# Performance work log

Hardware: AMD Instinct MI355X
Metric: run time of the kernel (lower is better)

Reference implementation:

```python
import jax, jax.numpy as jnp
import numpy as np

N_NODES, N_EDGES, P, C, H = 10000, 80000, 4, 128, 8
D = C // H


def setup_inputs() -> dict:
    key = jax.random.key(0)
    ks = jax.random.split(key, 24)

    def lin(k, i, o):
        return (jax.random.normal(k, (i, o), jnp.float32) / np.sqrt(i)).astype(jnp.float32)

    return {
        'h': jax.random.normal(ks[0], (N_NODES, P, C), jnp.float32),
        'e': jax.random.normal(ks[1], (N_EDGES, P, C), jnp.float32),
        'src': jax.random.randint(ks[2], (N_EDGES,), 0, N_NODES),
        'dst': jax.random.randint(ks[3], (N_EDGES,), 0, N_NODES),
        # MultiHeadAttentionLayer (use_bias=False)
        'Wq': lin(ks[4], C, C), 'Wk': lin(ks[5], C, C), 'Wv': lin(ks[6], C, C), 'We': lin(ks[7], C, C),
        # EnhanceLayer (bias=False)
        'eWq': lin(ks[8], C, C), 'eWk': lin(ks[9], C, C), 'eWv': lin(ks[10], C, C), 'eWre': lin(ks[11], C, C),
        # output projections
        'Oh_w': lin(ks[12], C, C), 'Oh_b': jnp.zeros((C,), jnp.float32),
        'Oe_w': lin(ks[13], C, C), 'Oe_b': jnp.zeros((C,), jnp.float32),
        # batch-norm affine params (training-mode stats)
        'bn_h_g': jnp.ones((C,), jnp.float32), 'bn_h_b': jnp.zeros((C,), jnp.float32),
        'bn_e_g': jnp.ones((C,), jnp.float32), 'bn_e_b': jnp.zeros((C,), jnp.float32),
        # FFN for h
        'W1': lin(ks[14], C, 2 * C), 'b1': jnp.zeros((2 * C,), jnp.float32),
        'W2': lin(ks[15], 2 * C, C), 'b2': jnp.zeros((C,), jnp.float32),
    }


def _forward(h, e, src, dst, Wq, Wk, Wv, We, eWq, eWk, eWv, eWre,
             Oh_w, Oh_b, Oe_w, Oe_b, bn_h_g, bn_h_b, bn_e_g, bn_e_b,
             W1, b1, W2, b2):
    n_nodes, p, c = h.shape
    n_edges = src.shape[0]
    d = c // H

    def heads(x):
        return x.reshape(x.shape[0], p, H, d)

    # ---- MultiHeadAttentionLayer.propagate_attention ----
    Q = heads(h @ Wq)          # (n, P, H, D)
    K = heads(h @ Wk)
    V = heads(h @ Wv)
    proj_e = heads(e @ We)     # (E, P, H, D)

    # src_dot_dst -> scaling -> relative_pe_attn
    score = (K[src] * Q[dst]) / jnp.sqrt(jnp.float32(d)) + proj_e  # (E, P, H, D)
    e_out = score                                                  # out_edge_features('score')
    s = jnp.exp(jnp.clip(score.sum(-1, keepdims=True), -5.0, 5.0))  # (E, P, H, 1)

    wV = jax.ops.segment_sum(V[src] * s, dst, num_segments=n_nodes)  # (n, P, H, D)
    z = jax.ops.segment_sum(s, dst, num_segments=n_nodes)            # (n, P, H, 1)
    h_attn = wV / (z + 1e-6)

    # ---- EnhanceLayer.propagate_attention ----
    Qe = heads(h @ eWq)
    diff = jax.nn.relu(h[src] - h[dst])             # (E, P, C)
    k_diff = heads(diff @ eWk)                      # (E, P, H, D)
    v_diff = heads(diff @ eWv)
    repe = heads(e @ eWre)
    qd = Qe[dst]
    # dst_cosim_diff: (q*k) * (||k||*||q|| + 1e-6) + repe   (eps in sqrt for grad safety)
    nk = jnp.sqrt(jnp.sum(k_diff * k_diff, -1, keepdims=True) + 1e-12)
    nq = jnp.sqrt(jnp.sum(qd * qd, -1, keepdims=True) + 1e-12)
    sc = qd * k_diff * (nk * nq + 1e-6) + repe
    msg = sc * v_diff
    h_enh = jax.ops.segment_max(msg, dst, num_segments=n_nodes)
    h_enh = jnp.where(jnp.isfinite(h_enh), h_enh, 0.0)  # DGL zero-fills nodes with no in-edges

    # ---- combine, project, residual, BN, FFN (dropout=0) ----
    hf = (h_attn + h_enh).reshape(n_nodes * p, c)
    ef = e_out.reshape(n_edges * p, c)
    hf = hf @ Oh_w + Oh_b
    ef = ef @ Oe_w + Oe_b
    hf = h.reshape(-1, c) + hf   # residual
    ef = e.reshape(-1, c) + ef

    def bn(x, g, b):
        m = x.mean(0)
        v = x.var(0)
        return (x - m) * jax.lax.rsqrt(v + 1e-5) * g + b

    hf = bn(hf, bn_h_g, bn_h_b)
    ef = bn(ef, bn_e_g, bn_e_b)

    h2 = hf
    hf = jax.nn.relu(hf @ W1 + b1) @ W2 + b2
    hf = h2 + hf
    return hf.reshape(n_nodes, p, c), ef.reshape(n_edges, p, c)


def reference(h, e, src, dst, Wq, Wk, Wv, We, eWq, eWk, eWv, eWre,
              Oh_w, Oh_b, Oe_w, Oe_b, bn_h_g, bn_h_b, bn_e_g, bn_e_b,
              W1, b1, W2, b2):
    return _forward(h, e, src, dst, Wq, Wk, Wv, We, eWq, eWk, eWv, eWre,
                    Oh_w, Oh_b, Oe_w, Oe_b, bn_h_g, bn_h_b, bn_e_g, bn_e_b,
                    W1, b1, W2, b2)
```

## Files before the change

kernel.cpp:

```cpp
#include <hip/hip_runtime.h>
#include <hip/hip_bf16.h>

#define NN 10000
#define NE 80000
#define PP 4
#define CC 128
#define NR (NN*PP)
#define ER (NE*PP)
#define S1 136
#define S2 264

typedef unsigned short u16;
typedef unsigned int   u32;
typedef __attribute__((ext_vector_type(8))) short short8;
typedef __attribute__((ext_vector_type(4))) float f32x4;

__device__ inline float b2f(u16 v) { return __uint_as_float(((u32)v) << 16); }
__device__ inline u16 f2b(float f) {
    u32 x = __float_as_uint(f);
    return (u16)((x + 0x7fffu + ((x >> 16) & 1u)) >> 16);
}
__device__ inline void atomicMaxF(float* addr, float val) {
    if (val >= 0.f) atomicMax((int*)addr, __float_as_int(val));
    else            atomicMin((u32*)addr, __float_as_uint(val));
}
__device__ inline f32x4 mfma16(short8 a, short8 b, f32x4 c) {
    return __builtin_amdgcn_mfma_f32_16x16x32_bf16(a, b, c, 0, 0, 0);
}

__global__ __launch_bounds__(512) void k_qkvqe(const float* __restrict__ h,
    const float* __restrict__ Wq, const float* __restrict__ Wk,
    const float* __restrict__ Wv, const float* __restrict__ eWq,
    float* __restrict__ out)
{
    __shared__ __align__(16) u16 hH[64 * S1];
    __shared__ __align__(16) u16 hL[64 * S1];
    const int t = threadIdx.x;
    const int lane = t & 63;
    const int wid = t >> 6;
    const int lrow = lane & 15;
    const int lgrp = lane >> 4;

    short8 wf[4][4];
#pragma unroll
    for (int nt = 0; nt < 4; ++nt) {
        int col = wid * 64 + nt * 16 + lrow;
        int sel = col >> 7, wc = col & 127;
        const float* W = (sel == 0) ? Wq : (sel == 1) ? Wk : (sel == 2) ? Wv : eWq;
#pragma unroll
        for (int ks = 0; ks < 4; ++ks) {
            short8 a;
#pragma unroll
            for (int j = 0; j < 8; ++j) {
                int k = ks * 32 + lgrp * 8 + j;
                a[j] = (short)f2b(W[k * 128 + wc]);
            }
            wf[nt][ks] = a;
        }
    }

    const int nTiles = NR / 64;
    for (int tl = blockIdx.x; tl < nTiles; tl += gridDim.x) {
        const int rbase = tl * 64;
        {
            int r = t >> 3, c0 = (t & 7) * 16;
            const float4* h4 = (const float4*)(h + (size_t)(rbase + r) * 128 + c0);
            u32* HH = (u32*)(hH + r * S1 + c0);
            u32* HL = (u32*)(hL + r * S1 + c0);
#pragma unroll
            for (int q2 = 0; q2 < 4; ++q2) {
                float4 v = h4[q2];
                u16 h0 = f2b(v.x), h1 = f2b(v.y), h2 = f2b(v.z), h3 = f2b(v.w);
                HH[q2 * 2]     = (u32)h0 | ((u32)h1 << 16);
                HH[q2 * 2 + 1] = (u32)h2 | ((u32)h3 << 16);
                u16 l0 = f2b(v.x - b2f(h0)), l1 = f2b(v.y - b2f(h1));
                u16 l2 = f2b(v.z - b2f(h2)), l3 = f2b(v.w - b2f(h3));
                HL[q2 * 2]     = (u32)l0 | ((u32)l1 << 16);
                HL[q2 * 2 + 1] = (u32)l2 | ((u32)l3 << 16);
            }
        }
        __syncthreads();
#pragma unroll
        for (int mt = 0; mt < 4; ++mt) {
            short8 Hh[4], Hl[4];
#pragma unroll
            for (int ks = 0; ks < 4; ++ks) {
                const int off = (mt * 16 + lrow) * S1 + ks * 32 + lgrp * 8;
                Hh[ks] = *(const short8*)(hH + off);
                Hl[ks] = *(const short8*)(hL + off);
            }
#pragma unroll
            for (int nt = 0; nt < 4; ++nt) {
                f32x4 acc = {0.f, 0.f, 0.f, 0.f};
#pragma unroll
                for (int ks = 0; ks < 4; ++ks) {
                    acc = mfma16(Hh[ks], wf[nt][ks], acc);
                    acc = mfma16(Hl[ks], wf[nt][ks], acc);
                }
#pragma unroll
                for (int q = 0; q < 4; ++q) {
                    int r = rbase + mt * 16 + lgrp * 4 + q;
                    out[(size_t)r * 512 + wid * 64 + nt * 16 + lrow] = acc[q];
                }
            }
        }
        __syncthreads();
    }
}

__global__ __launch_bounds__(512, 4) void k_attn(const float* __restrict__ e,
    const int* __restrict__ src, const int* __restrict__ dst,
    const float* __restrict__ We, const float* __restrict__ Oe_w, const float* __restrict__ Oe_b,
    const float* __restrict__ qkvqe, float* __restrict__ wV, float* __restrict__ z,
    float* __restrict__ stats, float* __restrict__ out_e)
{
    __shared__ __align__(16) u16 eH[64 * S1];
    __shared__ __align__(16) u16 eL[64 * S1];
    __shared__ int drowS[64], srowS[64];

    const int t = threadIdx.x;
    const int lane = t & 63;
    const int wid = t >> 6;
    const int lrow = lane & 15;
    const int lgrp = lane >> 4;
    const int c = wid * 16 + lrow;

    short8 we8[4], oe8[4];
#pragma unroll
    for (int ks = 0; ks < 4; ++ks) {
        short8 a, b;
#pragma unroll
        for (int j = 0; j < 8; ++j) {
            int k = ks * 32 + lgrp * 8 + j;
            int idx = k * 128 + c;
            a[j] = (short)f2b(We[idx]);
            b[j] = (short)f2b(Oe_w[idx]);
        }
        we8[ks] = a; oe8[ks] = b;
    }
    const float oeb = Oe_b[c];
    float s1 = 0.f, s2 = 0.f;

    const int nTiles = ER / 64;
    for (int tl = blockIdx.x; tl < nTiles; tl += gridDim.x) {
        const int rbase = tl * 64;
        {
            int r = t >> 3, c0 = (t & 7) * 16;
            int re = rbase + r, ei = re >> 2, p = re & 3;
            if ((t & 7) == 0) { drowS[r] = dst[ei] * 4 + p; srowS[r] = src[ei] * 4 + p; }
            const float4* ee4 = (const float4*)(e + (size_t)re * 128 + c0);
            u32* EH = (u32*)(eH + r * S1 + c0);
            u32* EL = (u32*)(eL + r * S1 + c0);
#pragma unroll
            for (int q2 = 0; q2 < 4; ++q2) {
                float4 ev = ee4[q2];
                u16 e0 = f2b(ev.x), e1 = f2b(ev.y), e2 = f2b(ev.z), e3 = f2b(ev.w);
                EH[q2 * 2]     = (u32)e0 | ((u32)e1 << 16);
                EH[q2 * 2 + 1] = (u32)e2 | ((u32)e3 << 16);
                u16 g0 = f2b(ev.x - b2f(e0)), g1 = f2b(ev.y - b2f(e1));
                u16 g2 = f2b(ev.z - b2f(e2)), g3 = f2b(ev.w - b2f(e3));
                EL[q2 * 2]     = (u32)g0 | ((u32)g1 << 16);
                EL[q2 * 2 + 1] = (u32)g2 | ((u32)g3 << 16);
            }
        }
        __syncthreads();

        f32x4 ap0 = {0.f,0.f,0.f,0.f}, ap1 = {0.f,0.f,0.f,0.f};
        f32x4 ap2 = {0.f,0.f,0.f,0.f}, ap3 = {0.f,0.f,0.f,0.f};
#pragma unroll
        for (int ks = 0; ks < 4; ++ks) {
            const int boff = ks * 32 + lgrp * 8;
            ap0 = mfma16(*(const short8*)(eH + (0 * 16 + lrow) * S1 + boff), we8[ks], ap0);
            ap0 = mfma16(*(const short8*)(eL + (0 * 16 + lrow) * S1 + boff), we8[ks], ap0);
            ap1 = mfma16(*(const short8*)(eH + (1 * 16 + lrow) * S1 + boff), we8[ks], ap1);
            ap1 = mfma16(*(const short8*)(eL + (1 * 16 + lrow) * S1 + boff), we8[ks], ap1);
            ap2 = mfma16(*(const short8*)(eH + (2 * 16 + lrow) * S1 + boff), we8[ks], ap2);
            ap2 = mfma16(*(const short8*)(eL + (2 * 16 + lrow) * S1 + boff), we8[ks], ap2);
            ap3 = mfma16(*(const short8*)(eH + (3 * 16 + lrow) * S1 + boff), we8[ks], ap3);
            ap3 = mfma16(*(const short8*)(eL + (3 * 16 + lrow) * S1 + boff), we8[ks], ap3);
        }
        __syncthreads();

        float evr[16];
#pragma unroll
        for (int mt = 0; mt < 4; ++mt) {
            int dr4[4], sr4[4];
#pragma unroll
            for (int q = 0; q < 4; ++q) {
                int rr = mt * 16 + lgrp * 4 + q;
                dr4[q] = drowS[rr]; sr4[q] = srowS[rr];
            }
            float kg[4], qg[4], vg[4];
#pragma unroll
            for (int q = 0; q < 4; ++q) {
                kg[q] = qkvqe[(size_t)sr4[q] * 512 + 128 + c];
                qg[q] = qkvqe[(size_t)dr4[q] * 512 + c];
                vg[q] = qkvqe[(size_t)sr4[q] * 512 + 256 + c];
            }
            f32x4 ap = (mt == 0) ? ap0 : (mt == 1) ? ap1 : (mt == 2) ? ap2 : ap3;
#pragma unroll
            for (int q = 0; q < 4; ++q) {
                int rr = mt * 16 + lgrp * 4 + q;
                float scv = kg[q] * qg[q] * 0.25f + ap[q];
                float hs = scv;
                hs += __shfl_xor(hs, 1); hs += __shfl_xor(hs, 2);
                hs += __shfl_xor(hs, 4); hs += __shfl_xor(hs, 8);
                hs = fminf(fmaxf(hs, -5.f), 5.f);
                float sv = expf(hs);
                if (lrow == 0) atomicAdd(&z[dr4[q] * 8 + wid], sv);
                atomicAdd(&wV[(size_t)dr4[q] * 128 + c], vg[q] * sv);
                int off2 = rr * S1 + c;
                evr[mt * 4 + q] = b2f(eH[off2]) + b2f(eL[off2]);
                u16 shh = f2b(scv);
                eH[off2] = shh;
                eL[off2] = f2b(scv - b2f(shh));
            }
        }
        __syncthreads();

#pragma unroll
        for (int mt = 0; mt < 4; ++mt) {
            f32x4 ao = {0.f, 0.f, 0.f, 0.f};
#pragma unroll
            for (int ks = 0; ks < 4; ++ks) {
                const int off = (mt * 16 + lrow) * S1 + ks * 32 + lgrp * 8;
                ao = mfma16(*(const short8*)(eH + off), oe8[ks], ao);
                ao = mfma16(*(const short8*)(eL + off), oe8[ks], ao);
            }
#pragma unroll
            for (int q = 0; q < 4; ++q) {
                int rr = mt * 16 + lgrp * 4 + q;
                int re = rbase + rr;
                float ef = evr[mt * 4 + q] + oeb + ao[q];
                out_e[(size_t)re * 128 + c] = ef;
                s1 += ef; s2 += ef * ef;
            }
        }
        __syncthreads();
    }
    atomicAdd(&stats[256 + c], s1);
    atomicAdd(&stats[384 + c], s2);
}

__global__ __launch_bounds__(512) void k_enh(const float* __restrict__ h, const float* __restrict__ e,
    const int* __restrict__ src, const int* __restrict__ dst,
    const float* __restrict__ eWk, const float* __restrict__ eWv, const float* __restrict__ eWre,
    const float* __restrict__ qkvqe, float* __restrict__ henh)
{
    __shared__ __align__(16) u16 diffH[64 * S1];
    __shared__ __align__(16) u16 diffL[64 * S1];
    __shared__ __align__(16) u16 erH[64 * S1];
    __shared__ __align__(16) u16 erL[64 * S1];
    __shared__ int drowS[64];

    const int t = threadIdx.x;
    const int lane = t & 63;
    const int wid = t >> 6;
    const int lrow = lane & 15;
    const int lgrp = lane >> 4;

    short8 wkh[4], wkl[4], wv8[4], wre8[4];
#pragma unroll
    for (int ks = 0; ks < 4; ++ks) {
        short8 a, b, c2, d2;
#pragma unroll
        for (int j = 0; j < 8; ++j) {
            int k = ks * 32 + lgrp * 8 + j;
            int idx = k * 128 + wid * 16 + lrow;
            float wk = eWk[idx];
            u16 hh = f2b(wk);
            a[j]  = (short)hh;
            b[j]  = (short)f2b(wk - b2f(hh));
            c2[j] = (short)f2b(eWv[idx]);
            d2[j] = (short)f2b(eWre[idx]);
        }
        wkh[ks] = a; wkl[ks] = b; wv8[ks] = c2; wre8[ks] = d2;
    }

    const int nTiles = ER / 64;
    for (int tl = blockIdx.x; tl < nTiles; tl += gridDim.x) {
        const int rbase = tl * 64;
        {
            int r = t >> 3, c0 = (t & 7) * 16;
            int re = rbase + r, ei = re >> 2, p = re & 3;
            int sr = src[ei] * 4 + p, dr = dst[ei] * 4 + p;
            if ((t & 7) == 0) drowS[r] = dr;
            const float4* hs4 = (const float4*)(h + (size_t)sr * 128 + c0);
            const float4* hd4 = (const float4*)(h + (size_t)dr * 128 + c0);
            const float4* ee4 = (const float4*)(e + (size_t)re * 128 + c0);
            u32* dH = (u32*)(diffH + r * S1 + c0);
            u32* dL = (u32*)(diffL + r * S1 + c0);
            u32* eH = (u32*)(erH + r * S1 + c0);
            u32* eL = (u32*)(erL + r * S1 + c0);
#pragma unroll
            for (int q2 = 0; q2 < 4; ++q2) {
                float4 a = hs4[q2], b = hd4[q2], ev = ee4[q2];
                float d0 = fmaxf(a.x - b.x, 0.f), d1 = fmaxf(a.y - b.y, 0.f);
                float d2 = fmaxf(a.z - b.z, 0.f), d3 = fmaxf(a.w - b.w, 0.f);
                u16 h0 = f2b(d0), h1 = f2b(d1), h2 = f2b(d2), h3 = f2b(d3);
                dH[q2 * 2]     = (u32)h0 | ((u32)h1 << 16);
                dH[q2 * 2 + 1] = (u32)h2 | ((u32)h3 << 16);
                u16 l0 = f2b(d0 - b2f(h0)), l1 = f2b(d1 - b2f(h1));
                u16 l2 = f2b(d2 - b2f(h2)), l3 = f2b(d3 - b2f(h3));
                dL[q2 * 2]     = (u32)l0 | ((u32)l1 << 16);
                dL[q2 * 2 + 1] = (u32)l2 | ((u32)l3 << 16);
                u16 e0 = f2b(ev.x), e1 = f2b(ev.y), e2 = f2b(ev.z), e3 = f2b(ev.w);
                eH[q2 * 2]     = (u32)e0 | ((u32)e1 << 16);
                eH[q2 * 2 + 1] = (u32)e2 | ((u32)e3 << 16);
                u16 g0 = f2b(ev.x - b2f(e0)), g1 = f2b(ev.y - b2f(e1));
                u16 g2 = f2b(ev.z - b2f(e2)), g3 = f2b(ev.w - b2f(e3));
                eL[q2 * 2]     = (u32)g0 | ((u32)g1 << 16);
                eL[q2 * 2 + 1] = (u32)g2 | ((u32)g3 << 16);
            }
        }
        __syncthreads();

#pragma unroll
        for (int mt = 0; mt < 4; ++mt) {
            f32x4 ak = {0.f, 0.f, 0.f, 0.f};
            f32x4 av = {0.f, 0.f, 0.f, 0.f};
            f32x4 ar = {0.f, 0.f, 0.f, 0.f};
#pragma unroll
            for (int ks = 0; ks < 4; ++ks) {
                const int off = (mt * 16 + lrow) * S1 + ks * 32 + lgrp * 8;
                short8 Ah = *(const short8*)(diffH + off);
                short8 Al = *(const short8*)(diffL + off);
                short8 Eh = *(const short8*)(erH + off);
                short8 El = *(const short8*)(erL + off);
                ak = mfma16(Ah, wkh[ks], ak);
                ak = mfma16(Al, wkh[ks], ak);
                ak = mfma16(Ah, wkl[ks], ak);
                av = mfma16(Ah, wv8[ks], av);
                av = mfma16(Al, wv8[ks], av);
                ar = mfma16(Eh, wre8[ks], ar);
                ar = mfma16(El, wre8[ks], ar);
            }
#pragma unroll
            for (int q = 0; q < 4; ++q) {
                int rr = mt * 16 + lgrp * 4 + q;
                int dr = drowS[rr];
                float qd = qkvqe[(size_t)dr * 512 + 384 + wid * 16 + lrow];
                float kd = ak[q];
                float sk = kd * kd;
                sk += __shfl_xor(sk, 1); sk += __shfl_xor(sk, 2);
                sk += __shfl_xor(sk, 4); sk += __shfl_xor(sk, 8);
                float sq = qd * qd;
                sq += __shfl_xor(sq, 1); sq += __shfl_xor(sq, 2);
                sq += __shfl_xor(sq, 4); sq += __shfl_xor(sq, 8);
                float nk = sqrtf(sk + 1e-12f);
                float nq = sqrtf(sq + 1e-12f);
                float sc = qd * kd * (nk * nq + 1e-6f) + ar[q];
                float msg = sc * av[q];
                atomicMaxF(&henh[(size_t)dr * 128 + wid * 16 + lrow], msg);
            }
        }
        __syncthreads();
    }
}

__global__ __launch_bounds__(512, 8) void k_comb(const float* __restrict__ h,
    const float* __restrict__ Oh_w, const float* __restrict__ Oh_b,
    const float* __restrict__ wV, const float* __restrict__ z, const float* __restrict__ henh,
    float* __restrict__ hf, float* __restrict__ stats)
{
    __shared__ __align__(16) u16 xH[64 * S1];
    __shared__ __align__(16) u16 xL[64 * S1];
    const int t = threadIdx.x;
    const int lane = t & 63;
    const int wid = t >> 6;
    const int lrow = lane & 15;
    const int lgrp = lane >> 4;
    const int c = wid * 16 + lrow;

    short8 oh8[4];
#pragma unroll
    for (int ks = 0; ks < 4; ++ks) {
        short8 a;
#pragma unroll
        for (int j = 0; j < 8; ++j) {
            int k = ks * 32 + lgrp * 8 + j;
            a[j] = (short)f2b(Oh_w[k * 128 + c]);
        }
        oh8[ks] = a;
    }
    const float ohb = Oh_b[c];
    float s1 = 0.f, s2 = 0.f;

    const int nTiles = NR / 64;
    for (int tl = blockIdx.x; tl < nTiles; tl += gridDim.x) {
        const int rbase = tl * 64;
        {
            int r = t >> 3, c0 = (t & 7) * 16;
            int gr = rbase + r;
            float zv = z[gr * 8 + (t & 7)] + 1e-6f;
            const float4* wv4 = (const float4*)(wV + (size_t)gr * 128 + c0);
            const float4* he4 = (const float4*)(henh + (size_t)gr * 128 + c0);
            u32* XH = (u32*)(xH + r * S1 + c0);
            u32* XL = (u32*)(xL + r * S1 + c0);
#pragma unroll
            for (int q2 = 0; q2 < 4; ++q2) {
                float4 a = wv4[q2], b = he4[q2];
                float x0, x1, x2, x3;
                {
                    u32 hb = __float_as_uint(b.x); float hv = (((hb >> 23) & 0xffu) == 0xffu) ? 0.f : b.x;
                    x0 = a.x / zv + hv;
                }
                {
                    u32 hb = __float_as_uint(b.y); float hv = (((hb >> 23) & 0xffu) == 0xffu) ? 0.f : b.y;
                    x1 = a.y / zv + hv;
                }
                {
                    u32 hb = __float_as_uint(b.z); float hv = (((hb >> 23) & 0xffu) == 0xffu) ? 0.f : b.z;
                    x2 = a.z / zv + hv;
                }
                {
                    u32 hb = __float_as_uint(b.w); float hv = (((hb >> 23) & 0xffu) == 0xffu) ? 0.f : b.w;
                    x3 = a.w / zv + hv;
                }
                u16 h0 = f2b(x0), h1 = f2b(x1), h2 = f2b(x2), h3 = f2b(x3);
                XH[q2 * 2]     = (u32)h0 | ((u32)h1 << 16);
                XH[q2 * 2 + 1] = (u32)h2 | ((u32)h3 << 16);
                u16 l0 = f2b(x0 - b2f(h0)), l1 = f2b(x1 - b2f(h1));
                u16 l2 = f2b(x2 - b2f(h2)), l3 = f2b(x3 - b2f(h3));
                XL[q2 * 2]     = (u32)l0 | ((u32)l1 << 16);
                XL[q2 * 2 + 1] = (u32)l2 | ((u32)l3 << 16);
            }
        }
        __syncthreads();
#pragma unroll
        for (int mt = 0; mt < 4; ++mt) {
            f32x4 acc = {0.f, 0.f, 0.f, 0.f};
#pragma unroll
            for (int ks = 0; ks < 4; ++ks) {
                const int off = (mt * 16 + lrow) * S1 + ks * 32 + lgrp * 8;
                acc = mfma16(*(const short8*)(xH + off), oh8[ks], acc);
                acc = mfma16(*(const short8*)(xL + off), oh8[ks], acc);
            }
#pragma unroll
            for (int q = 0; q < 4; ++q) {
                int r = rbase + mt * 16 + lgrp * 4 + q;
                float val = h[(size_t)r * 128 + c] + ohb + acc[q];
                hf[(size_t)r * 128 + c] = val;
                s1 += val; s2 += val * val;
            }
        }
        __syncthreads();
    }
    atomicAdd(&stats[c], s1);
    atomicAdd(&stats[128 + c], s2);
}

__global__ void k_bnprep(const float* __restrict__ stats,
    const float* __restrict__ gh, const float* __restrict__ bh,
    const float* __restrict__ ge, const float* __restrict__ be, float* __restrict__ bnsc)
{
    int c = threadIdx.x;
    if (c < 128) {
        float m = stats[c] / (float)NR;
        float v = stats[128 + c] / (float)NR - m * m;
        float sc = gh[c] * rsqrtf(v + 1e-5f);
        bnsc[c] = sc; bnsc[128 + c] = bh[c] - m * sc;
        m = stats[256 + c] / (float)ER;
        v = stats[384 + c] / (float)ER - m * m;
        sc = ge[c] * rsqrtf(v + 1e-5f);
        bnsc[256 + c] = sc; bnsc[384 + c] = be[c] - m * sc;
    }
}

__global__ __launch_bounds__(512, 4) void k_ffn(const float* __restrict__ hf,
    const float* __restrict__ W1, const float* __restrict__ b1,
    const float* __restrict__ W2, const float* __restrict__ b2,
    const float* __restrict__ bnsc, float* __restrict__ out_h)
{
    __shared__ __align__(16) u16 xH[32 * S1];
    __shared__ __align__(16) u16 xL[32 * S1];
    __shared__ __align__(16) u16 tH[32 * S2];
    __shared__ __align__(16) u16 tL[32 * S2];
    __shared__ float scs[128], shs[128];
    const int t = threadIdx.x;
    const int lane = t & 63;
    const int wid = t >> 6;
    const int lrow = lane & 15;
    const int lgrp = lane >> 4;

    short8 w1f[2][4];
#pragma unroll
    for (int nt = 0; nt < 2; ++nt) {
        int col = wid * 32 + nt * 16 + lrow;
#pragma unroll
        for (int ks = 0; ks < 4; ++ks) {
            short8 a;
#pragma unroll
            for (int j = 0; j < 8; ++j) {
                int k = ks * 32 + lgrp * 8 + j;
                a[j] = (short)f2b(W1[k * 256 + col]);
            }
            w1f[nt][ks] = a;
        }
    }
    short8 w2f[8];
#pragma unroll
    for (int ks = 0; ks < 8; ++ks) {
        short8 a;
#pragma unroll
        for (int j = 0; j < 8; ++j) {
            int k = ks * 32 + lgrp * 8 + j;
            a[j] = (short)f2b(W2[k * 128 + wid * 16 + lrow]);
        }
        w2f[ks] = a;
    }
    const float bb1a = b1[wid * 32 + lrow];
    const float bb1b = b1[wid * 32 + 16 + lrow];
    const float bb2 = b2[wid * 16 + lrow];
    if (t < 128) { scs[t] = bnsc[t]; shs[t] = bnsc[128 + t]; }
    __syncthreads();

    const int nTiles = NR / 32;
    for (int tl = blockIdx.x; tl < nTiles; tl += gridDim.x) {
        const int rbase = tl * 32;
        {
            int r = t >> 4, c0 = (t & 15) * 8;
            const float4* s4 = (const float4*)(hf + (size_t)(rbase + r) * 128 + c0);
            u32* XH = (u32*)(xH + r * S1 + c0);
            u32* XL = (u32*)(xL + r * S1 + c0);
#pragma unroll
            for (int q2 = 0; q2 < 2; ++q2) {
                float4 v = s4[q2];
                float x0 = v.x * scs[c0 + q2 * 4 + 0] + shs[c0 + q2 * 4 + 0];
                float x1 = v.y * scs[c0 + q2 * 4 + 1] + shs[c0 + q2 * 4 + 1];
                float x2 = v.z * scs[c0 + q2 * 4 + 2] + shs[c0 + q2 * 4 + 2];
                float x3 = v.w * scs[c0 + q2 * 4 + 3] + shs[c0 + q2 * 4 + 3];
                u16 h0 = f2b(x0), h1 = f2b(x1), h2 = f2b(x2), h3 = f2b(x3);
                XH[q2 * 2]     = (u32)h0 | ((u32)h1 << 16);
                XH[q2 * 2 + 1] = (u32)h2 | ((u32)h3 << 16);
                u16 l0 = f2b(x0 - b2f(h0)), l1 = f2b(x1 - b2f(h1));
                u16 l2 = f2b(x2 - b2f(h2)), l3 = f2b(x3 - b2f(h3));
                XL[q2 * 2]     = (u32)l0 | ((u32)l1 << 16);
                XL[q2 * 2 + 1] = (u32)l2 | ((u32)l3 << 16);
            }
        }
        __syncthreads();
#pragma unroll
        for (int mt = 0; mt < 2; ++mt) {
#pragma unroll
            for (int nt = 0; nt < 2; ++nt) {
                f32x4 acc = {0.f, 0.f, 0.f, 0.f};
#pragma unroll
                for (int ks = 0; ks < 4; ++ks) {
                    const int off = (mt * 16 + lrow) * S1 + ks * 32 + lgrp * 8;
                    acc = mfma16(*(const short8*)(xH + off), w1f[nt][ks], acc);
                    acc = mfma16(*(const short8*)(xL + off), w1f[nt][ks], acc);
                }
                float bb = nt ? bb1b : bb1a;
                int col = wid * 32 + nt * 16 + lrow;
#pragma unroll
                for (int q = 0; q < 4; ++q) {
                    int rr = mt * 16 + lgrp * 4 + q;
                    float tv = fmaxf(acc[q] + bb, 0.f);
                    u16 hh = f2b(tv);
                    tH[rr * S2 + col] = hh;
                    tL[rr * S2 + col] = f2b(tv - b2f(hh));
                }
            }
        }
        __syncthreads();
#pragma unroll
        for (int mt = 0; mt < 2; ++mt) {
            f32x4 acc = {0.f, 0.f, 0.f, 0.f};
#pragma unroll
            for (int ks = 0; ks < 8; ++ks) {
                const int off = (mt * 16 + lrow) * S2 + ks * 32 + lgrp * 8;
                acc = mfma16(*(const short8*)(tH + off), w2f[ks], acc);
                acc = mfma16(*(const short8*)(tL + off), w2f[ks], acc);
            }
            int c2 = wid * 16 + lrow;
#pragma unroll
            for (int q = 0; q < 4; ++q) {
                int rr = mt * 16 + lgrp * 4 + q;
                int offx = rr * S1 + c2;
                float xn = b2f(xH[offx]) + b2f(xL[offx]);
                float o = xn + bb2 + acc[q];
                out_h[(size_t)(rbase + rr) * 128 + c2] = o;
            }
        }
        __syncthreads();
    }
}

__global__ __launch_bounds__(256) void k_bne(float* __restrict__ out_e, const float* __restrict__ bnsc)
{
    __shared__ float scs[128], shs[128];
    const int t = threadIdx.x;
    if (t < 128) { scs[t] = bnsc[256 + t]; shs[t] = bnsc[384 + t]; }
    __syncthreads();
    int idx = blockIdx.x * 256 + t;
    const int total = ER * 128 / 4;
    for (; idx < total; idx += gridDim.x * 256) {
        float4 v = ((const float4*)out_e)[idx];
        int c0 = (idx * 4) & 127;
        v.x = v.x * scs[c0 + 0] + shs[c0 + 0];
        v.y = v.y * scs[c0 + 1] + shs[c0 + 1];
        v.z = v.z * scs[c0 + 2] + shs[c0 + 2];
        v.w = v.w * scs[c0 + 3] + shs[c0 + 3];
        ((float4*)out_e)[idx] = v;
    }
}

extern "C" void kernel_launch(void* const* d_in, const int* in_sizes, int n_in,
                              void* d_out, int out_size, void* d_ws, size_t ws_size,
                              hipStream_t stream)
{
    const float* h    = (const float*)d_in[0];
    const float* e    = (const float*)d_in[1];
    const int* src    = (const int*)d_in[2];
    const int* dst    = (const int*)d_in[3];
    const float* Wq   = (const float*)d_in[4];
    const float* Wk   = (const float*)d_in[5];
    const float* Wv   = (const float*)d_in[6];
    const float* We   = (const float*)d_in[7];
    const float* eWq  = (const float*)d_in[8];
    const float* eWk  = (const float*)d_in[9];
    const float* eWv  = (const float*)d_in[10];
    const float* eWre = (const float*)d_in[11];
    const float* Oh_w = (const float*)d_in[12];
    const float* Oh_b = (const float*)d_in[13];
    const float* Oe_w = (const float*)d_in[14];
    const float* Oe_b = (const float*)d_in[15];
    const float* bnhg = (const float*)d_in[16];
    const float* bnhb = (const float*)d_in[17];
    const float* bneg = (const float*)d_in[18];
    const float* bneb = (const float*)d_in[19];
    const float* W1   = (const float*)d_in[20];
    const float* b1   = (const float*)d_in[21];
    const float* W2   = (const float*)d_in[22];
    const float* b2   = (const float*)d_in[23];

    float* out_h = (float*)d_out;
    float* out_e = out_h + (size_t)NR * 128;

    char* w = (char*)d_ws;
    float* qkvqe = (float*)(w);
    float* wV    = (float*)(w + 81920000);
    float* z     = (float*)(w + 102400000);
    float* henh  = (float*)(w + 103680000);
    float* hf    = (float*)(w + 124160000);
    float* stats = (float*)(w + 144640000);
    float* bnsc  = (float*)(w + 144642048);

    hipMemsetAsync(wV,    0,    20480000, stream);
    hipMemsetAsync(z,     0,    1280000,  stream);
    hipMemsetAsync(stats, 0,    2048,     stream);
    hipMemsetAsync(henh,  0xFF, 20480000, stream);

    k_qkvqe<<<625, 512, 0, stream>>>(h, Wq, Wk, Wv, eWq, qkvqe);
    k_attn <<<1024, 512, 0, stream>>>(e, src, dst, We, Oe_w, Oe_b, qkvqe, wV, z, stats, out_e);
    k_enh  <<<1024, 512, 0, stream>>>(h, e, src, dst, eWk, eWv, eWre, qkvqe, henh);
    k_comb <<<625, 512, 0, stream>>>(h, Oh_w, Oh_b, wV, z, henh, hf, stats);
    k_bnprep<<<1, 128, 0, stream>>>(stats, bnhg, bnhb, bneg, bneb, bnsc);
    k_ffn  <<<1250, 512, 0, stream>>>(hf, W1, b1, W2, b2, bnsc, out_h);
    k_bne  <<<2048, 256, 0, stream>>>(out_e, bnsc);
}
```

Before: 1.582 ms.

## Merge attention and enhance edge kernels into one launch with block-parity split

The two edge-pass kernels are combined into one kernel. Even blocks run the attention/score path and odd blocks run the enhance/segment-max path, so both independent workloads run at the same time on the GPU and fill idle tail slots. Grid size changes to 2000 (1000 blocks per path). The cost is higher shared-memory use (four buffers in every block, which the attention blocks do not need), and this may lower occupancy for the attention half.

```diff
diff --git a/kernel.cpp b/kernel.cpp
--- a/kernel.cpp
+++ b/kernel.cpp
@@ -108,14 +108,18 @@
     }
 }
 
-__global__ __launch_bounds__(512, 4) void k_attn(const float* __restrict__ e,
+__global__ __launch_bounds__(512, 4) void k_edge(
+    const float* __restrict__ h, const float* __restrict__ e,
     const int* __restrict__ src, const int* __restrict__ dst,
     const float* __restrict__ We, const float* __restrict__ Oe_w, const float* __restrict__ Oe_b,
+    const float* __restrict__ eWk, const float* __restrict__ eWv, const float* __restrict__ eWre,
     const float* __restrict__ qkvqe, float* __restrict__ wV, float* __restrict__ z,
-    float* __restrict__ stats, float* __restrict__ out_e)
+    float* __restrict__ stats, float* __restrict__ out_e, float* __restrict__ henh)
 {
-    __shared__ __align__(16) u16 eH[64 * S1];
-    __shared__ __align__(16) u16 eL[64 * S1];
+    __shared__ __align__(16) u16 bAH[64 * S1];
+    __shared__ __align__(16) u16 bAL[64 * S1];
+    __shared__ __align__(16) u16 bBH[64 * S1];
+    __shared__ __align__(16) u16 bBL[64 * S1];
     __shared__ int drowS[64], srowS[64];
 
     const int t = threadIdx.x;
@@ -124,237 +128,222 @@
     const int lrow = lane & 15;
     const int lgrp = lane >> 4;
     const int c = wid * 16 + lrow;
-
-    short8 we8[4], oe8[4];
-#pragma unroll
-    for (int ks = 0; ks < 4; ++ks) {
-        short8 a, b;
-#pragma unroll
-        for (int j = 0; j < 8; ++j) {
-            int k = ks * 32 + lgrp * 8 + j;
-            int idx = k * 128 + c;
-            a[j] = (short)f2b(We[idx]);
-            b[j] = (short)f2b(Oe_w[idx]);
-        }
-        we8[ks] = a; oe8[ks] = b;
-    }
-    const float oeb = Oe_b[c];
-    float s1 = 0.f, s2 = 0.f;
-
+    const int bstream = blockIdx.x >> 1;
     const int nTiles = ER / 64;
-    for (int tl = blockIdx.x; tl < nTiles; tl += gridDim.x) {
-        const int rbase = tl * 64;
-        {
-            int r = t >> 3, c0 = (t & 7) * 16;
-            int re = rbase + r, ei = re >> 2, p = re & 3;
-            if ((t & 7) == 0) { drowS[r] = dst[ei] * 4 + p; srowS[r] = src[ei] * 4 + p; }
-            const float4* ee4 = (const float4*)(e + (size_t)re * 128 + c0);
-            u32* EH = (u32*)(eH + r * S1 + c0);
-            u32* EL = (u32*)(eL + r * S1 + c0);
-#pragma unroll
-            for (int q2 = 0; q2 < 4; ++q2) {
-                float4 ev = ee4[q2];
-                u16 e0 = f2b(ev.x), e1 = f2b(ev.y), e2 = f2b(ev.z), e3 = f2b(ev.w);
-                EH[q2 * 2]     = (u32)e0 | ((u32)e1 << 16);
-                EH[q2 * 2 + 1] = (u32)e2 | ((u32)e3 << 16);
-                u16 g0 = f2b(ev.x - b2f(e0)), g1 = f2b(ev.y - b2f(e1));
-                u16 g2 = f2b(ev.z - b2f(e2)), g3 = f2b(ev.w - b2f(e3));
-                EL[q2 * 2]     = (u32)g0 | ((u32)g1 << 16);
-                EL[q2 * 2 + 1] = (u32)g2 | ((u32)g3 << 16);
-            }
-        }
-        __syncthreads();
-
-        f32x4 ap0 = {0.f,0.f,0.f,0.f}, ap1 = {0.f,0.f,0.f,0.f};
-        f32x4 ap2 = {0.f,0.f,0.f,0.f}, ap3 = {0.f,0.f,0.f,0.f};
+    const int bstride = gridDim.x >> 1;
+
+    if ((blockIdx.x & 1) == 0) {
+        short8 we8[4], oe8[4];
 #pragma unroll
         for (int ks = 0; ks < 4; ++ks) {
-            const int boff = ks * 32 + lgrp * 8;
-            ap0 = mfma16(*(const short8*)(eH + (0 * 16 + lrow) * S1 + boff), we8[ks], ap0);
-            ap0 = mfma16(*(const short8*)(eL + (0 * 16 + lrow) * S1 + boff), we8[ks], ap0);
-            ap1 = mfma16(*(const short8*)(eH + (1 * 16 + lrow) * S1 + boff), we8[ks], ap1);
-            ap1 = mfma16(*(const short8*)(eL + (1 * 16 + lrow) * S1 + boff), we8[ks], ap1);
-            ap2 = mfma16(*(const short8*)(eH + (2 * 16 + lrow) * S1 + boff), we8[ks], ap2);
-            ap2 = mfma16(*(const short8*)(eL + (2 * 16 + lrow) * S1 + boff), we8[ks], ap2);
-            ap3 = mfma16(*(const short8*)(eH + (3 * 16 + lrow) * S1 + boff), we8[ks], ap3);
-            ap3 = mfma16(*(const short8*)(eL + (3 * 16 + lrow) * S1 + boff), we8[ks], ap3);
-        }
-        __syncthreads();
-
-        float evr[16];
-#pragma unroll
-        for (int mt = 0; mt < 4; ++mt) {
-            int dr4[4], sr4[4];
-#pragma unroll
-            for (int q = 0; q < 4; ++q) {
-                int rr = mt * 16 + lgrp * 4 + q;
-                dr4[q] = drowS[rr]; sr4[q] = srowS[rr];
-            }
-            float kg[4], qg[4], vg[4];
-#pragma unroll
-            for (int q = 0; q < 4; ++q) {
-                kg[q] = qkvqe[(size_t)sr4[q] * 512 + 128 + c];
-                qg[q] = qkvqe[(size_t)dr4[q] * 512 + c];
-                vg[q] = qkvqe[(size_t)sr4[q] * 512 + 256 + c];
-            }
-            f32x4 ap = (mt == 0) ? ap0 : (mt == 1) ? ap1 : (mt == 2) ? ap2 : ap3;
-#pragma unroll
-            for (int q = 0; q < 4; ++q) {
-                int rr = mt * 16 + lgrp * 4 + q;
-                float scv = kg[q] * qg[q] * 0.25f + ap[q];
-                float hs = scv;
-                hs += __shfl_xor(hs, 1); hs += __shfl_xor(hs, 2);
-                hs += __shfl_xor(hs, 4); hs += __shfl_xor(hs, 8);
-                hs = fminf(fmaxf(hs, -5.f), 5.f);
-                float sv = expf(hs);
-                if (lrow == 0) atomicAdd(&z[dr4[q] * 8 + wid], sv);
-                atomicAdd(&wV[(size_t)dr4[q] * 128 + c], vg[q] * sv);
-                int off2 = rr * S1 + c;
-                evr[mt * 4 + q] = b2f(eH[off2]) + b2f(eL[off2]);
-                u16 shh = f2b(scv);
-                eH[off2] = shh;
-                eL[off2] = f2b(scv - b2f(shh));
-            }
-        }
-        __syncthreads();
-
-#pragma unroll
-        for (int mt = 0; mt < 4; ++mt) {
-            f32x4 ao = {0.f, 0.f, 0.f, 0.f};
+            short8 a, b;
+#pragma unroll
+            for (int j = 0; j < 8; ++j) {
+                int k = ks * 32 + lgrp * 8 + j;
+                int idx = k * 128 + c;
+                a[j] = (short)f2b(We[idx]);
+                b[j] = (short)f2b(Oe_w[idx]);
+            }
+            we8[ks] = a; oe8[ks] = b;
+        }
+        const float oeb = Oe_b[c];
+        float s1 = 0.f, s2 = 0.f;
+
+        for (int tl = bstream; tl < nTiles; tl += bstride) {
+            const int rbase = tl * 64;
+            {
+                int r = t >> 3, c0 = (t & 7) * 16;
+                int re = rbase + r, ei = re >> 2, p = re & 3;
+                if ((t & 7) == 0) { drowS[r] = dst[ei] * 4 + p; srowS[r] = src[ei] * 4 + p; }
+                const float4* ee4 = (const float4*)(e + (size_t)re * 128 + c0);
+                u32* EH = (u32*)(bAH + r * S1 + c0);
+                u32* EL = (u32*)(bAL + r * S1 + c0);
+#pragma unroll
+                for (int q2 = 0; q2 < 4; ++q2) {
+                    float4 ev = ee4[q2];
+                    u16 e0 = f2b(ev.x), e1 = f2b(ev.y), e2 = f2b(ev.z), e3 = f2b(ev.w);
+                    EH[q2 * 2]     = (u32)e0 | ((u32)e1 << 16);
+                    EH[q2 * 2 + 1] = (u32)e2 | ((u32)e3 << 16);
+                    u16 g0 = f2b(ev.x - b2f(e0)), g1 = f2b(ev.y - b2f(e1));
+                    u16 g2 = f2b(ev.z - b2f(e2)), g3 = f2b(ev.w - b2f(e3));
+                    EL[q2 * 2]     = (u32)g0 | ((u32)g1 << 16);
+                    EL[q2 * 2 + 1] = (u32)g2 | ((u32)g3 << 16);
+                }
+            }
+            __syncthreads();
+
+            f32x4 ap0 = {0.f,0.f,0.f,0.f}, ap1 = {0.f,0.f,0.f,0.f};
+            f32x4 ap2 = {0.f,0.f,0.f,0.f}, ap3 = {0.f,0.f,0.f,0.f};
 #pragma unroll
             for (int ks = 0; ks < 4; ++ks) {
-                const int off = (mt * 16 + lrow) * S1 + ks * 32 + lgrp * 8;
-                ao = mfma16(*(const short8*)(eH + off), oe8[ks], ao);
-                ao = mfma16(*(const short8*)(eL + off), oe8[ks], ao);
-            }
-#pragma unroll
-            for (int q = 0; q < 4; ++q) {
-                int rr = mt * 16 + lgrp * 4 + q;
-                int re = rbase + rr;
-                float ef = evr[mt * 4 + q] + oeb + ao[q];
-                out_e[(size_t)re * 128 + c] = ef;
-                s1 += ef; s2 += ef * ef;
-            }
-        }
-        __syncthreads();
-    }
-    atomicAdd(&stats[256 + c], s1);
-    atomicAdd(&stats[384 + c], s2);
-}
-
-__global__ __launch_bounds__(512) void k_enh(const float* __restrict__ h, const float* __restrict__ e,
-    const int* __restrict__ src, const int* __restrict__ dst,
-    const float* __restrict__ eWk, const float* __restrict__ eWv, const float* __restrict__ eWre,
-    const float* __restrict__ qkvqe, float* __restrict__ henh)
-{
-    __shared__ __align__(16) u16 diffH[64 * S1];
-    __shared__ __align__(16) u16 diffL[64 * S1];
-    __shared__ __align__(16) u16 erH[64 * S1];
-    __shared__ __align__(16) u16 erL[64 * S1];
-    __shared__ int drowS[64];
-
-    const int t = threadIdx.x;
-    const int lane = t & 63;
-    const int wid = t >> 6;
-    const int lrow = lane & 15;
-    const int lgrp = lane >> 4;
-
-    short8 wkh[4], wkl[4], wv8[4], wre8[4];
-#pragma unroll
-    for (int ks = 0; ks < 4; ++ks) {
-        short8 a, b, c2, d2;
-#pragma unroll
-        for (int j = 0; j < 8; ++j) {
-            int k = ks * 32 + lgrp * 8 + j;
-            int idx = k * 128 + wid * 16 + lrow;
-            float wk = eWk[idx];
-            u16 hh = f2b(wk);
-            a[j]  = (short)hh;
-            b[j]  = (short)f2b(wk - b2f(hh));
-            c2[j] = (short)f2b(eWv[idx]);
-            d2[j] = (short)f2b(eWre[idx]);
-        }
-        wkh[ks] = a; wkl[ks] = b; wv8[ks] = c2; wre8[ks] = d2;
-    }
-
-    const int nTiles = ER / 64;
-    for (int tl = blockIdx.x; tl < nTiles; tl += gridDim.x) {
-        const int rbase = tl * 64;
-        {
-            int r = t >> 3, c0 = (t & 7) * 16;
-            int re = rbase + r, ei = re >> 2, p = re & 3;
-            int sr = src[ei] * 4 + p, dr = dst[ei] * 4 + p;
-            if ((t & 7) == 0) drowS[r] = dr;
-            const float4* hs4 = (const float4*)(h + (size_t)sr * 128 + c0);
-            const float4* hd4 = (const float4*)(h + (size_t)dr * 128 + c0);
-            const float4* ee4 = (const float4*)(e + (size_t)re * 128 + c0);
-            u32* dH = (u32*)(diffH + r * S1 + c0);
-            u32* dL = (u32*)(diffL + r * S1 + c0);
-            u32* eH = (u32*)(erH + r * S1 + c0);
-            u32* eL = (u32*)(erL + r * S1 + c0);
-#pragma unroll
-            for (int q2 = 0; q2 < 4; ++q2) {
-                float4 a = hs4[q2], b = hd4[q2], ev = ee4[q2];
-                float d0 = fmaxf(a.x - b.x, 0.f), d1 = fmaxf(a.y - b.y, 0.f);
-                float d2 = fmaxf(a.z - b.z, 0.f), d3 = fmaxf(a.w - b.w, 0.f);
-                u16 h0 = f2b(d0), h1 = f2b(d1), h2 = f2b(d2), h3 = f2b(d3);
-                dH[q2 * 2]     = (u32)h0 | ((u32)h1 << 16);
-                dH[q2 * 2 + 1] = (u32)h2 | ((u32)h3 << 16);
-                u16 l0 = f2b(d0 - b2f(h0)), l1 = f2b(d1 - b2f(h1));
-                u16 l2 = f2b(d2 - b2f(h2)), l3 = f2b(d3 - b2f(h3));
-                dL[q2 * 2]     = (u32)l0 | ((u32)l1 << 16);
-                dL[q2 * 2 + 1] = (u32)l2 | ((u32)l3 << 16);
-                u16 e0 = f2b(ev.x), e1 = f2b(ev.y), e2 = f2b(ev.z), e3 = f2b(ev.w);
-                eH[q2 * 2]     = (u32)e0 | ((u32)e1 << 16);
-                eH[q2 * 2 + 1] = (u32)e2 | ((u32)e3 << 16);
-                u16 g0 = f2b(ev.x - b2f(e0)), g1 = f2b(ev.y - b2f(e1));
-                u16 g2 = f2b(ev.z - b2f(e2)), g3 = f2b(ev.w - b2f(e3));
-                eL[q2 * 2]     = (u32)g0 | ((u32)g1 << 16);
-                eL[q2 * 2 + 1] = (u32)g2 | ((u32)g3 << 16);
-            }
-        }
-        __syncthreads();
-
-#pragma unroll
-        for (int mt = 0; mt < 4; ++mt) {
-            f32x4 ak = {0.f, 0.f, 0.f, 0.f};
-            f32x4 av = {0.f, 0.f, 0.f, 0.f};
-            f32x4 ar = {0.f, 0.f, 0.f, 0.f};
-#pragma unroll
-            for (int ks = 0; ks < 4; ++ks) {
-                const int off = (mt * 16 + lrow) * S1 + ks * 32 + lgrp * 8;
-                short8 Ah = *(const short8*)(diffH + off);
-                short8 Al = *(const short8*)(diffL + off);
-                short8 Eh = *(const short8*)(erH + off);
-                short8 El = *(const short8*)(erL + off);
-                ak = mfma16(Ah, wkh[ks], ak);
-                ak = mfma16(Al, wkh[ks], ak);
-                ak = mfma16(Ah, wkl[ks], ak);
-                av = mfma16(Ah, wv8[ks], av);
-                av = mfma16(Al, wv8[ks], av);
-                ar = mfma16(Eh, wre8[ks], ar);
-                ar = mfma16(El, wre8[ks], ar);
-            }
-#pragma unroll
-            for (int q = 0; q < 4; ++q) {
-                int rr = mt * 16 + lgrp * 4 + q;
-                int dr = drowS[rr];
-                float qd = qkvqe[(size_t)dr * 512 + 384 + wid * 16 + lrow];
-                float kd = ak[q];
-                float sk = kd * kd;
-                sk += __shfl_xor(sk, 1); sk += __shfl_xor(sk, 2);
-                sk += __shfl_xor(sk, 4); sk += __shfl_xor(sk, 8);
-                float sq = qd * qd;
-                sq += __shfl_xor(sq, 1); sq += __shfl_xor(sq, 2);
-                sq += __shfl_xor(sq, 4); sq += __shfl_xor(sq, 8);
-                float nk = sqrtf(sk + 1e-12f);
-                float nq = sqrtf(sq + 1e-12f);
-                float sc = qd * kd * (nk * nq + 1e-6f) + ar[q];
-                float msg = sc * av[q];
-                atomicMaxF(&henh[(size_t)dr * 128 + wid * 16 + lrow], msg);
-            }
-        }
-        __syncthreads();
+                const int boff = ks * 32 + lgrp * 8;
+                ap0 = mfma16(*(const short8*)(bAH + (0 * 16 + lrow) * S1 + boff), we8[ks], ap0);
+                ap0 = mfma16(*(const short8*)(bAL + (0 * 16 + lrow) * S1 + boff), we8[ks], ap0);
+                ap1 = mfma16(*(const short8*)(bAH + (1 * 16 + lrow) * S1 + boff), we8[ks], ap1);
+                ap1 = mfma16(*(const short8*)(bAL + (1 * 16 + lrow) * S1 + boff), we8[ks], ap1);
+                ap2 = mfma16(*(const short8*)(bAH + (2 * 16 + lrow) * S1 + boff), we8[ks], ap2);
+                ap2 = mfma16(*(const short8*)(bAL + (2 * 16 + lrow) * S1 + boff), we8[ks], ap2);
+                ap3 = mfma16(*(const short8*)(bAH + (3 * 16 + lrow) * S1 + boff), we8[ks], ap3);
+                ap3 = mfma16(*(const short8*)(bAL + (3 * 16 + lrow) * S1 + boff), we8[ks], ap3);
+            }
+            __syncthreads();
+
+            float evr[16];
+#pragma unroll
+            for (int mt = 0; mt < 4; ++mt) {
+                int dr4[4], sr4[4];
+#pragma unroll
+                for (int q = 0; q < 4; ++q) {
+                    int rr = mt * 16 + lgrp * 4 + q;
+                    dr4[q] = drowS[rr]; sr4[q] = srowS[rr];
+                }
+                float kg[4], qg[4], vg[4];
+#pragma unroll
+                for (int q = 0; q < 4; ++q) {
+                    kg[q] = qkvqe[(size_t)sr4[q] * 512 + 128 + c];
+                    qg[q] = qkvqe[(size_t)dr4[q] * 512 + c];
+                    vg[q] = qkvqe[(size_t)sr4[q] * 512 + 256 + c];
+                }
+                f32x4 ap = (mt == 0) ? ap0 : (mt == 1) ? ap1 : (mt == 2) ? ap2 : ap3;
+#pragma unroll
+                for (int q = 0; q < 4; ++q) {
+                    int rr = mt * 16 + lgrp * 4 + q;
+                    float scv = kg[q] * qg[q] * 0.25f + ap[q];
+                    float hs = scv;
+                    hs += __shfl_xor(hs, 1); hs += __shfl_xor(hs, 2);
+                    hs += __shfl_xor(hs, 4); hs += __shfl_xor(hs, 8);
+                    hs = fminf(fmaxf(hs, -5.f), 5.f);
+                    float sv = expf(hs);
+                    if (lrow == 0) atomicAdd(&z[dr4[q] * 8 + wid], sv);
+                    atomicAdd(&wV[(size_t)dr4[q] * 128 + c], vg[q] * sv);
+                    int off2 = rr * S1 + c;
+                    evr[mt * 4 + q] = b2f(bAH[off2]) + b2f(bAL[off2]);
+                    u16 shh = f2b(scv);
+                    bAH[off2] = shh;
+                    bAL[off2] = f2b(scv - b2f(shh));
+                }
+            }
+            __syncthreads();
+
+#pragma unroll
+            for (int mt = 0; mt < 4; ++mt) {
+                f32x4 ao = {0.f, 0.f, 0.f, 0.f};
+#pragma unroll
+                for (int ks = 0; ks < 4; ++ks) {
+                    const int off = (mt * 16 + lrow) * S1 + ks * 32 + lgrp * 8;
+                    ao = mfma16(*(const short8*)(bAH + off), oe8[ks], ao);
+                    ao = mfma16(*(const short8*)(bAL + off), oe8[ks], ao);
+                }
+#pragma unroll
+                for (int q = 0; q < 4; ++q) {
+                    int rr = mt * 16 + lgrp * 4 + q;
+                    int re = rbase + rr;
+                    float ef = evr[mt * 4 + q] + oeb + ao[q];
+                    out_e[(size_t)re * 128 + c] = ef;
+                    s1 += ef; s2 += ef * ef;
+                }
+            }
+            __syncthreads();
+        }
+        atomicAdd(&stats[256 + c], s1);
+        atomicAdd(&stats[384 + c], s2);
+    } else {
+        short8 wkh[4], wkl[4], wv8[4], wre8[4];
+#pragma unroll
+        for (int ks = 0; ks < 4; ++ks) {
+            short8 a, b, c2, d2;
+#pragma unroll
+            for (int j = 0; j < 8; ++j) {
+                int k = ks * 32 + lgrp * 8 + j;
+                int idx = k * 128 + c;
+                float wk = eWk[idx];
+                u16 hh = f2b(wk);
+                a[j]  = (short)hh;
+                b[j]  = (short)f2b(wk - b2f(hh));
+                c2[j] = (short)f2b(eWv[idx]);
+                d2[j] = (short)f2b(eWre[idx]);
+            }
+            wkh[ks] = a; wkl[ks] = b; wv8[ks] = c2; wre8[ks] = d2;
+        }
+
+        for (int tl = bstream; tl < nTiles; tl += bstride) {
+            const int rbase = tl * 64;
+            {
+                int r = t >> 3, c0 = (t & 7) * 16;
+                int re = rbase + r, ei = re >> 2, p = re & 3;
+                int sr = src[ei] * 4 + p, dr = dst[ei] * 4 + p;
+                if ((t & 7) == 0) drowS[r] = dr;
+                const float4* hs4 = (const float4*)(h + (size_t)sr * 128 + c0);
+                const float4* hd4 = (const float4*)(h + (size_t)dr * 128 + c0);
+                const float4* ee4 = (const float4*)(e + (size_t)re * 128 + c0);
+                u32* dH = (u32*)(bAH + r * S1 + c0);
+                u32* dL = (u32*)(bAL + r * S1 + c0);
+                u32* eH = (u32*)(bBH + r * S1 + c0);
+                u32* eL = (u32*)(bBL + r * S1 + c0);
+#pragma unroll
+                for (int q2 = 0; q2 < 4; ++q2) {
+                    float4 a = hs4[q2], b = hd4[q2], ev = ee4[q2];
+                    float d0 = fmaxf(a.x - b.x, 0.f), d1 = fmaxf(a.y - b.y, 0.f);
+                    float d2 = fmaxf(a.z - b.z, 0.f), d3 = fmaxf(a.w - b.w, 0.f);
+                    u16 h0 = f2b(d0), h1 = f2b(d1), h2 = f2b(d2), h3 = f2b(d3);
+                    dH[q2 * 2]     = (u32)h0 | ((u32)h1 << 16);
+                    dH[q2 * 2 + 1] = (u32)h2 | ((u32)h3 << 16);
+                    u16 l0 = f2b(d0 - b2f(h0)), l1 = f2b(d1 - b2f(h1));
+                    u16 l2 = f2b(d2 - b2f(h2)), l3 = f2b(d3 - b2f(h3));
+                    dL[q2 * 2]     = (u32)l0 | ((u32)l1 << 16);
+                    dL[q2 * 2 + 1] = (u32)l2 | ((u32)l3 << 16);
+                    u16 e0 = f2b(ev.x), e1 = f2b(ev.y), e2 = f2b(ev.z), e3 = f2b(ev.w);
+                    eH[q2 * 2]     = (u32)e0 | ((u32)e1 << 16);
+                    eH[q2 * 2 + 1] = (u32)e2 | ((u32)e3 << 16);
+                    u16 g0 = f2b(ev.x - b2f(e0)), g1 = f2b(ev.y - b2f(e1));
+                    u16 g2 = f2b(ev.z - b2f(e2)), g3 = f2b(ev.w - b2f(e3));
+                    eL[q2 * 2]     = (u32)g0 | ((u32)g1 << 16);
+                    eL[q2 * 2 + 1] = (u32)g2 | ((u32)g3 << 16);
+                }
+            }
+            __syncthreads();
+
+#pragma unroll
+            for (int mt = 0; mt < 4; ++mt) {
+                f32x4 ak = {0.f, 0.f, 0.f, 0.f};
+                f32x4 av = {0.f, 0.f, 0.f, 0.f};
+                f32x4 ar = {0.f, 0.f, 0.f, 0.f};
+#pragma unroll
+                for (int ks = 0; ks < 4; ++ks) {
+                    const int off = (mt * 16 + lrow) * S1 + ks * 32 + lgrp * 8;
+                    short8 Ah = *(const short8*)(bAH + off);
+                    short8 Al = *(const short8*)(bAL + off);
+                    short8 Eh = *(const short8*)(bBH + off);
+                    short8 El = *(const short8*)(bBL + off);
+                    ak = mfma16(Ah, wkh[ks], ak);
+                    ak = mfma16(Al, wkh[ks], ak);
+                    ak = mfma16(Ah, wkl[ks], ak);
+                    av = mfma16(Ah, wv8[ks], av);
+                    av = mfma16(Al, wv8[ks], av);
+                    ar = mfma16(Eh, wre8[ks], ar);
+                    ar = mfma16(El, wre8[ks], ar);
+                }
+#pragma unroll
+                for (int q = 0; q < 4; ++q) {
+                    int rr = mt * 16 + lgrp * 4 + q;
+                    int dr = drowS[rr];
+                    float qd = qkvqe[(size_t)dr * 512 + 384 + c];
+                    float kd = ak[q];
+                    float sk = kd * kd;
+                    sk += __shfl_xor(sk, 1); sk += __shfl_xor(sk, 2);
+                    sk += __shfl_xor(sk, 4); sk += __shfl_xor(sk, 8);
+                    float sq = qd * qd;
+                    sq += __shfl_xor(sq, 1); sq += __shfl_xor(sq, 2);
+                    sq += __shfl_xor(sq, 4); sq += __shfl_xor(sq, 8);
+                    float nk = sqrtf(sk + 1e-12f);
+                    float nq = sqrtf(sq + 1e-12f);
+                    float sc = qd * kd * (nk * nq + 1e-6f) + ar[q];
+                    float msg = sc * av[q];
+                    atomicMaxF(&henh[(size_t)dr * 128 + c], msg);
+                }
+            }
+            __syncthreads();
+        }
     }
 }
 
@@ -653,8 +642,8 @@
     hipMemsetAsync(henh,  0xFF, 20480000, stream);
 
     k_qkvqe<<<625, 512, 0, stream>>>(h, Wq, Wk, Wv, eWq, qkvqe);
-    k_attn <<<1024, 512, 0, stream>>>(e, src, dst, We, Oe_w, Oe_b, qkvqe, wV, z, stats, out_e);
-    k_enh  <<<1024, 512, 0, stream>>>(h, e, src, dst, eWk, eWv, eWre, qkvqe, henh);
+    k_edge <<<2000, 512, 0, stream>>>(h, e, src, dst, We, Oe_w, Oe_b, eWk, eWv, eWre,
+                                      qkvqe, wV, z, stats, out_e, henh);
     k_comb <<<625, 512, 0, stream>>>(h, Oh_w, Oh_b, wV, z, henh, hf, stats);
     k_bnprep<<<1, 128, 0, stream>>>(stats, bnhg, bnhb, bneg, bneb, bnsc);
     k_ffn  <<<1250, 512, 0, stream>>>(hf, W1, b1, W2, b2, bnsc, out_h);
```

Measured after the change: 1.475 ms. 1.07x faster.
